# Kernel tuning notes

Hardware: AMD Instinct MI355X
Metric: run time of the kernel (lower is better)

The kernel has to match this reference:

```python
import jax, jax.numpy as jnp
import numpy as np
from jax.ops import segment_sum, segment_max

N = 20000      # nodes
DEG = 16       # incoming edges per node
E = N * DEG    # edges
IN = 128       # in_features
BOND = 16      # bond_features_dim
OUT = 128      # output_features
NUM_LAYERS = 3
LEAKY = 0.2
ELU_ALPHA = 1.0


def _lin_params(key, out_f, in_f):
    kw, kb = jax.random.split(key)
    s = 1.0 / np.sqrt(in_f)
    w = jax.random.uniform(kw, (out_f, in_f), jnp.float32, -s, s)
    b = jax.random.uniform(kb, (out_f,), jnp.float32, -s, s)
    return w, b


def setup_inputs() -> dict:
    key = jax.random.key(0)
    ks = jax.random.split(key, 20)
    atom_features = jax.random.normal(ks[0], (N, IN), jnp.float32)
    edge_src = jax.random.randint(ks[1], (E,), 0, N, jnp.int32)
    # every node receives exactly DEG edges (avoids the isolated-node bug path)
    edge_dst = jnp.repeat(jnp.arange(N, dtype=jnp.int32), DEG)
    bond_features = jax.random.normal(ks[2], (E, BOND), jnp.float32)

    v1_fc1_w, v1_fc1_b = _lin_params(ks[3], OUT, IN)
    v1_fc2_w, v1_fc2_b = _lin_params(ks[4], OUT, IN + BOND)
    v1_att_w, v1_att_b = _lin_params(ks[5], 1, 2 * OUT)
    v1_attend_w, v1_attend_b = _lin_params(ks[6], OUT, OUT)
    v1_gru_wih, v1_gru_bih = _lin_params(ks[7], 3 * OUT, OUT)
    v1_gru_whh, v1_gru_bhh = _lin_params(ks[8], 3 * OUT, OUT)

    v2_fc1_w, v2_fc1_b = _lin_params(ks[9], 1, 2 * OUT)
    v2_fc2_w, v2_fc2_b = _lin_params(ks[10], OUT, OUT)
    v2_gru_wih, v2_gru_bih = _lin_params(ks[11], 3 * OUT, OUT)
    v2_gru_whh, v2_gru_bhh = _lin_params(ks[12], 3 * OUT, OUT)

    lin_w, lin_b = _lin_params(ks[13], OUT, OUT)

    return dict(atom_features=atom_features, edge_src=edge_src, edge_dst=edge_dst,
                bond_features=bond_features,
                v1_fc1_w=v1_fc1_w, v1_fc1_b=v1_fc1_b, v1_fc2_w=v1_fc2_w, v1_fc2_b=v1_fc2_b,
                v1_att_w=v1_att_w, v1_att_b=v1_att_b, v1_attend_w=v1_attend_w, v1_attend_b=v1_attend_b,
                v1_gru_wih=v1_gru_wih, v1_gru_whh=v1_gru_whh, v1_gru_bih=v1_gru_bih, v1_gru_bhh=v1_gru_bhh,
                v2_fc1_w=v2_fc1_w, v2_fc1_b=v2_fc1_b, v2_fc2_w=v2_fc2_w, v2_fc2_b=v2_fc2_b,
                v2_gru_wih=v2_gru_wih, v2_gru_whh=v2_gru_whh, v2_gru_bih=v2_gru_bih, v2_gru_bhh=v2_gru_bhh,
                lin_w=lin_w, lin_b=lin_b)


def _linear(x, w, b):
    return x @ w.T + b


def _gru_cell(x, h, wih, whh, bih, bhh):
    gi = x @ wih.T + bih   # [N, 3*OUT]
    gh = h @ whh.T + bhh
    i_r, i_z, i_n = jnp.split(gi, 3, axis=-1)
    h_r, h_z, h_n = jnp.split(gh, 3, axis=-1)
    r = jax.nn.sigmoid(i_r + h_r)
    z = jax.nn.sigmoid(i_z + h_z)
    n = jnp.tanh(i_n + r * h_n)
    return (1.0 - z) * n + z * h


def _segment_softmax(logits, seg, n):
    m = segment_max(logits, seg, num_segments=n)
    ex = jnp.exp(logits - m[seg])
    den = segment_sum(ex, seg, num_segments=n)
    return ex / den[seg]


def reference(atom_features, edge_src, edge_dst, bond_features,
              v1_fc1_w, v1_fc1_b, v1_fc2_w, v1_fc2_b, v1_att_w, v1_att_b,
              v1_attend_w, v1_attend_b, v1_gru_wih, v1_gru_whh, v1_gru_bih, v1_gru_bhh,
              v2_fc1_w, v2_fc1_b, v2_fc2_w, v2_fc2_b,
              v2_gru_wih, v2_gru_whh, v2_gru_bih, v2_gru_bhh,
              lin_w, lin_b):
    n = atom_features.shape[0]
    lrelu = lambda x: jax.nn.leaky_relu(x, negative_slope=LEAKY)

    # ---- GATlayerV1 ----
    new_atom = lrelu(_linear(atom_features, v1_fc1_w, v1_fc1_b))           # [N, OUT]
    nbr_trans = _linear(new_atom, v1_attend_w, v1_attend_b)                # [N, OUT]
    nbr_in = jnp.concatenate([atom_features[edge_src], bond_features], axis=1)  # [E, IN+BOND]
    nbr = lrelu(_linear(nbr_in, v1_fc2_w, v1_fc2_b))                       # [E, OUT]
    pair = jnp.concatenate([new_atom[edge_dst], nbr], axis=1)              # [E, 2*OUT]
    logits = lrelu(_linear(pair, v1_att_w, v1_att_b))[:, 0]                # [E]
    score = _segment_softmax(logits, edge_dst, n)                          # [E]
    transform = segment_sum(score[:, None] * nbr_trans[edge_src], edge_dst, num_segments=n)
    ctx = jax.nn.elu(transform, alpha=ELU_ALPHA)
    h = _gru_cell(ctx, new_atom, v1_gru_wih, v1_gru_whh, v1_gru_bih, v1_gru_bhh)
    G_0 = new_atom

    all_tensors = [h]

    # ---- GATlayerV2 (shared weights across layers 2..NUM_LAYERS) ----
    for _ in range(NUM_LAYERS - 1):
        nt = _linear(h, v2_fc2_w, v2_fc2_b)                                # [N, OUT]
        pair2 = jnp.concatenate([h[edge_dst], h[edge_src]], axis=1)        # [E, 2*OUT]
        lg = lrelu(_linear(pair2, v2_fc1_w, v2_fc1_b))[:, 0]               # [E]
        sc = _segment_softmax(lg, edge_dst, n)
        tr = segment_sum(sc[:, None] * nt[edge_src], edge_dst, num_segments=n)
        ctx2 = jax.nn.elu(tr, alpha=ELU_ALPHA)
        h = _gru_cell(ctx2, h, v2_gru_wih, v2_gru_whh, v2_gru_bih, v2_gru_bhh)
        all_tensors.append(h)

    all_stack = jnp.stack(all_tensors)           # [NUM_LAYERS, N, OUT]
    averaged = all_stack.mean(axis=0)            # [N, OUT]
    output = jax.nn.gelu(_linear(averaged, lin_w, lin_b), approximate=False)
    return (output, all_stack, G_0, averaged)
```

## Files before the change

kernel.cpp:

```cpp
#include <hip/hip_runtime.h>
#include <math.h>

#define NN 20000
#define EE 320000

using short8 = __attribute__((ext_vector_type(8))) short;
using f32x4  = __attribute__((ext_vector_type(4))) float;
using u16x4  = __attribute__((ext_vector_type(4))) unsigned short;

__device__ __forceinline__ unsigned short f2bf(float x) {
    union { float f; unsigned u; } v; v.f = x;
    unsigned r = (v.u + 0x7fffu + ((v.u >> 16) & 1u)) >> 16;
    return (unsigned short)r;
}
__device__ __forceinline__ float bf2f(unsigned short b) {
    union { unsigned u; float f; } v; v.u = ((unsigned)b) << 16;
    return v.f;
}
__device__ __forceinline__ float sigmoidf_(float x) { return 1.f / (1.f + __expf(-x)); }
__device__ __forceinline__ float tanhf_(float x) {
    float e = __expf(-2.f * x);
    return (1.f - e) / (1.f + e);
}
__device__ __forceinline__ float lrelu_(float x) { return x > 0.f ? x : 0.2f * x; }
__device__ __forceinline__ float elu_(float x) { return x > 0.f ? x : __expf(x) - 1.f; }

struct PackDesc { const float* w; unsigned short* out; int O; int ldw; int mode; };
struct PackArgs { PackDesc d[10]; };

__global__ void k_pack(PackArgs args) {
    PackDesc d = args.d[blockIdx.y];
    int idx = blockIdx.x * 256 + threadIdx.x;
    if (d.mode == 1) {
        if (idx >= 512) return;
        int t = idx >> 6, l = idx & 63;
        int lr = l & 15, lg = l >> 4;
        int ch = lr * 8 + t;
        short8 o;
        #pragma unroll
        for (int j = 0; j < 8; j++) {
            int k = lg * 8 + j;
            o[j] = (k < 16) ? (short)f2bf(d.w[(size_t)ch * 144 + 128 + k]) : (short)0;
        }
        *(short8*)(d.out + (size_t)idx * 8) = o;
        return;
    }
    int total = (d.O / 16) * 4 * 64;
    if (idx >= total) return;
    int l = idx & 63, rest = idx >> 6;
    int ko = rest & 3, no = rest >> 2;
    int row = no * 16 + (l & 15);
    int col0 = ko * 32 + ((l >> 4) * 8);
    const float* src = d.w + (size_t)row * d.ldw + col0;
    unsigned short o[8];
    #pragma unroll
    for (int j = 0; j < 8; j++) o[j] = f2bf(src[j]);
    #pragma unroll
    for (int j = 0; j < 8; j++) d.out[(size_t)idx * 8 + j] = o[j];
}

__global__ __launch_bounds__(256) void k_v1_front(
    const float* __restrict__ atom,
    const unsigned short* __restrict__ Bfc1, const unsigned short* __restrict__ BW2a,
    const float* __restrict__ fc1_b, const float* __restrict__ fc2_b,
    const float* __restrict__ attw,
    float* __restrict__ g0, unsigned short* __restrict__ naBf,
    unsigned short* __restrict__ Ubf, float* __restrict__ adst)
{
    __shared__ float Xs[16][132];
    __shared__ unsigned short Ys2[16 * 128];
    const int tid = threadIdx.x, l = tid & 63, w = tid >> 6;
    const int lr = l & 15, lg = l >> 4;
    const int m0 = blockIdx.x * 16;

    f32x4 acc1[2] = {}, accU[2] = {};
    #pragma unroll
    for (int ko = 0; ko < 4; ko++) {
        const f32x4* ap = (const f32x4*)(atom + (size_t)(m0 + lr) * 128 + ko * 32 + lg * 8);
        f32x4 a0 = ap[0], a1 = ap[1];
        short8 af;
        #pragma unroll
        for (int j = 0; j < 4; j++) { af[j] = (short)f2bf(a0[j]); af[4 + j] = (short)f2bf(a1[j]); }
        #pragma unroll
        for (int i = 0; i < 2; i++) {
            int t = w * 2 + i;
            short8 b1 = *(const short8*)(Bfc1 + ((size_t)(t * 4 + ko) * 64 + l) * 8);
            acc1[i] = __builtin_amdgcn_mfma_f32_16x16x32_bf16(af, b1, acc1[i], 0, 0, 0);
            short8 bu = *(const short8*)(BW2a + ((size_t)(t * 4 + ko) * 64 + l) * 8);
            accU[i] = __builtin_amdgcn_mfma_f32_16x16x32_bf16(af, bu, accU[i], 0, 0, 0);
        }
    }
    #pragma unroll
    for (int i = 0; i < 2; i++) {
        int col = (w * 2 + i) * 16 + lr;
        float b1v = fc1_b[col], bUv = fc2_b[col];
        #pragma unroll
        for (int r = 0; r < 4; r++) {
            int row = lg * 4 + r;
            float v = lrelu_(acc1[i][r] + b1v);
            Xs[row][col] = v;
            Ys2[row * 128 + col] = f2bf(accU[i][r] + bUv);
        }
    }
    __syncthreads();
    *(short8*)(Ubf + (size_t)m0 * 128 + tid * 8) = *(const short8*)(Ys2 + tid * 8);
    {
        int row = tid >> 4, q = tid & 15;
        short8 tmp;
        float p = 0.f;
        float vv[8];
        #pragma unroll
        for (int j = 0; j < 8; j++) {
            float x = Xs[row][q * 8 + j];
            vv[j] = x;
            tmp[j] = (short)f2bf(x);
            p = fmaf(x, attw[q * 8 + j], p);
        }
        *(f32x4*)(g0 + (size_t)(m0 + row) * 128 + q * 8) = *(f32x4*)vv;
        *(f32x4*)(g0 + (size_t)(m0 + row) * 128 + q * 8 + 4) = *(f32x4*)(vv + 4);
        *(short8*)(naBf + (size_t)(m0 + row) * 128 + q * 8) = tmp;
        #pragma unroll
        for (int m = 1; m <= 8; m <<= 1) p += __shfl_xor(p, m, 16);
        if (q == 0) adst[m0 + row] = p;
    }
}

__global__ __launch_bounds__(256) void k_logits_v1(
    const unsigned short* __restrict__ U, const int* __restrict__ esrc,
    const float* __restrict__ bond, const unsigned short* __restrict__ BW2b,
    const float* __restrict__ attw, const float* __restrict__ attb1,
    const float* __restrict__ adst, float* __restrict__ logits)
{
    const int tid = threadIdx.x, l = tid & 63, w = tid >> 6;
    const int lr = l & 15, lg = l >> 4;
    const int n = blockIdx.x * 4 + w;
    const int e0 = n * 16;

    short8 af = {};
    if (lg < 2) {
        const f32x4* bp = (const f32x4*)(bond + (size_t)(e0 + lr) * 16 + lg * 8);
        f32x4 b0 = bp[0], b1 = bp[1];
        #pragma unroll
        for (int j = 0; j < 4; j++) { af[j] = (short)f2bf(b0[j]); af[4 + j] = (short)f2bf(b1[j]); }
    }
    f32x4 c[8];
    #pragma unroll
    for (int t = 0; t < 8; t++) {
        short8 bf = *(const short8*)(BW2b + (size_t)(t * 64 + l) * 8);
        f32x4 z = {};
        c[t] = __builtin_amdgcn_mfma_f32_16x16x32_bf16(af, bf, z, 0, 0, 0);
    }
    float aw[8];
    #pragma unroll
    for (int t = 0; t < 8; t++) aw[t] = attw[128 + lr * 8 + t];

    float s[4];
    #pragma unroll
    for (int r = 0; r < 4; r++) {
        int e = e0 + lg * 4 + r;
        int src = esrc[e];
        short8 u = *(const short8*)(U + (size_t)src * 128 + lr * 8);
        float a0 = 0.f;
        #pragma unroll
        for (int t = 0; t < 8; t++)
            a0 = fmaf(aw[t], lrelu_(c[t][r] + bf2f((unsigned short)u[t])), a0);
        s[r] = a0;
    }
    #pragma unroll
    for (int mk = 1; mk <= 8; mk <<= 1)
        #pragma unroll
        for (int r = 0; r < 4; r++) s[r] += __shfl_xor(s[r], mk, 16);
    if (lr == 0) {
        float anode = adst[n], ab = attb1[0];
        f32x4 o;
        #pragma unroll
        for (int r = 0; r < 4; r++) o[r] = lrelu_(anode + ab + s[r]);
        *(f32x4*)(logits + e0 + lg * 4) = o;
    }
}

template<int AGGMODE, int FRONT, int FINAL>
__global__ __launch_bounds__(512, 4) void k_gru(
    const float* __restrict__ logits, const float* __restrict__ aD,
    const float* __restrict__ bS, const float* __restrict__ b1,
    const int* __restrict__ esrc, const unsigned short* __restrict__ V,
    const unsigned short* __restrict__ Bpre, const float* __restrict__ bpre,
    const unsigned short* __restrict__ Bih, const unsigned short* __restrict__ Bhh,
    const float* __restrict__ bih, const float* __restrict__ bhh,
    const unsigned short* __restrict__ hprevBf, float* __restrict__ houtF,
    unsigned short* __restrict__ houtBf,
    const float* __restrict__ w2att, float* __restrict__ aDOut, float* __restrict__ bSOut,
    const float* __restrict__ as0, const float* __restrict__ as1,
    const unsigned short* __restrict__ Blin, const float* __restrict__ linb,
    float* __restrict__ avgOut, float* __restrict__ outF)
{
    __shared__ unsigned short aggS[32][136];
    __shared__ unsigned short ctxS[32][136];
    __shared__ unsigned short hpS[32][136];
    __shared__ float hoS[32][132];
    const int tid = threadIdx.x, l = tid & 63, w = tid >> 6;
    const int lr = l & 15, lg = l >> 4;
    const int m0 = blockIdx.x * 32;
    const int srow = tid >> 4, sc0 = (tid & 15) * 8;

    *(short8*)&hpS[srow][sc0] = *(const short8*)(hprevBf + (size_t)(m0 + srow) * 128 + sc0);

    {
        const int q = tid & 15;
        const int gnode = m0 + srow;
        const int e = gnode * 16 + q;
        const int src = esrc[e];
        float lgt;
        if (AGGMODE == 0) lgt = logits[e];
        else              lgt = lrelu_(aD[gnode] + bS[src] + b1[0]);
        float mx = lgt;
        #pragma unroll
        for (int mk = 1; mk <= 8; mk <<= 1) mx = fmaxf(mx, __shfl_xor(mx, mk, 16));
        float ex = __expf(lgt - mx);
        float den = ex;
        #pragma unroll
        for (int mk = 1; mk <= 8; mk <<= 1) den += __shfl_xor(den, mk, 16);
        float wq = ex / den;
        float s[8] = {};
        #pragma unroll
        for (int i = 0; i < 16; i++) {
            float wi = __shfl(wq, i, 16);
            int si = __shfl(src, i, 16);
            const unsigned short* vp = V + (size_t)si * 128 + q * 4;
            u16x4 v0 = *(const u16x4*)vp;
            #pragma unroll
            for (int j = 0; j < 4; j++) s[j] = fmaf(wi, bf2f(v0[j]), s[j]);
            u16x4 v1 = *(const u16x4*)(vp + 64);
            #pragma unroll
            for (int j = 0; j < 4; j++) s[4 + j] = fmaf(wi, bf2f(v1[j]), s[4 + j]);
        }
        u16x4 o0, o1;
        #pragma unroll
        for (int j = 0; j < 4; j++) { o0[j] = f2bf(s[j]); o1[j] = f2bf(s[4 + j]); }
        *(u16x4*)&aggS[srow][q * 4] = o0;
        *(u16x4*)&aggS[srow][64 + q * 4] = o1;
    }
    __syncthreads();

    f32x4 accp[2] = {};
    #pragma unroll
    for (int ko = 0; ko < 4; ko++) {
        short8 bf = *(const short8*)(Bpre + ((size_t)(w * 4 + ko) * 64 + l) * 8);
        #pragma unroll
        for (int rt = 0; rt < 2; rt++) {
            short8 af = *(const short8*)&aggS[rt * 16 + lr][ko * 32 + lg * 8];
            accp[rt] = __builtin_amdgcn_mfma_f32_16x16x32_bf16(af, bf, accp[rt], 0, 0, 0);
        }
    }
    {
        const int col = w * 16 + lr;
        const float bb = bpre[col];
        #pragma unroll
        for (int rt = 0; rt < 2; rt++)
            #pragma unroll
            for (int r = 0; r < 4; r++)
                ctxS[rt * 16 + lg * 4 + r][col] = f2bf(elu_(accp[rt][r] + bb));
    }
    __syncthreads();

    f32x4 ai[2][3] = {}, ah[2][3] = {};
    #pragma unroll
    for (int ko = 0; ko < 4; ko++) {
        short8 afc[2], afh[2];
        #pragma unroll
        for (int rt = 0; rt < 2; rt++) {
            afc[rt] = *(const short8*)&ctxS[rt * 16 + lr][ko * 32 + lg * 8];
            afh[rt] = *(const short8*)&hpS[rt * 16 + lr][ko * 32 + lg * 8];
        }
        #pragma unroll
        for (int g = 0; g < 3; g++) {
            short8 bi = *(const short8*)(Bih + ((size_t)((w + 8 * g) * 4 + ko) * 64 + l) * 8);
            #pragma unroll
            for (int rt = 0; rt < 2; rt++)
                ai[rt][g] = __builtin_amdgcn_mfma_f32_16x16x32_bf16(afc[rt], bi, ai[rt][g], 0, 0, 0);
            short8 bh = *(const short8*)(Bhh + ((size_t)((w + 8 * g) * 4 + ko) * 64 + l) * 8);
            #pragma unroll
            for (int rt = 0; rt < 2; rt++)
                ah[rt][g] = __builtin_amdgcn_mfma_f32_16x16x32_bf16(afh[rt], bh, ah[rt][g], 0, 0, 0);
        }
    }
    __syncthreads();

    {
        const int c = w * 16 + lr;
        const float br = bih[c] + bhh[c];
        const float bz = bih[c + 128] + bhh[c + 128];
        const float bin_ = bih[c + 256];
        const float bhn = bhh[c + 256];
        #pragma unroll
        for (int rt = 0; rt < 2; rt++)
            #pragma unroll
            for (int r = 0; r < 4; r++) {
                const int lrow = rt * 16 + lg * 4 + r;
                float rg = sigmoidf_(ai[rt][0][r] + ah[rt][0][r] + br);
                float zg = sigmoidf_(ai[rt][1][r] + ah[rt][1][r] + bz);
                float ng = tanhf_(ai[rt][2][r] + bin_ + rg * (ah[rt][2][r] + bhn));
                float hp = bf2f(hpS[lrow][c]);
                hoS[lrow][c] = fmaf(zg, hp - ng, ng);
            }
    }
    __syncthreads();

    {
        float v[8];
        #pragma unroll
        for (int k = 0; k < 8; k++) v[k] = hoS[srow][sc0 + k];
        f32x4* dst = (f32x4*)(houtF + (size_t)(m0 + srow) * 128 + sc0);
        dst[0] = *(f32x4*)v;
        dst[1] = *(f32x4*)(v + 4);
        if (FINAL == 0) {
            short8 p;
            #pragma unroll
            for (int k = 0; k < 8; k++) p[k] = (short)f2bf(v[k]);
            *(short8*)(houtBf + (size_t)(m0 + srow) * 128 + sc0) = p;
        }
    }

    if (FRONT) {
        int row = tid >> 4, q = tid & 15;
        float pa = 0.f, pb = 0.f;
        #pragma unroll
        for (int j = 0; j < 8; j++) {
            float x = hoS[row][q * 8 + j];
            pa = fmaf(x, w2att[q * 8 + j], pa);
            pb = fmaf(x, w2att[128 + q * 8 + j], pb);
        }
        #pragma unroll
        for (int m = 1; m <= 8; m <<= 1) {
            pa += __shfl_xor(pa, m, 16);
            pb += __shfl_xor(pb, m, 16);
        }
        if (q == 0) { aDOut[m0 + row] = pa; bSOut[m0 + row] = pb; }
    }

    if (FINAL) {
        {
            const f32x4* p0 = (const f32x4*)(as0 + (size_t)(m0 + srow) * 128 + sc0);
            const f32x4* p1 = (const f32x4*)(as1 + (size_t)(m0 + srow) * 128 + sc0);
            f32x4* pav = (f32x4*)(avgOut + (size_t)(m0 + srow) * 128 + sc0);
            #pragma unroll
            for (int k = 0; k < 2; k++) {
                f32x4 x0 = p0[k], x1 = p1[k];
                f32x4 av;
                #pragma unroll
                for (int j = 0; j < 4; j++)
                    av[j] = (x0[j] + x1[j] + hoS[srow][sc0 + k * 4 + j]) * (1.f / 3.f);
                pav[k] = av;
                #pragma unroll
                for (int j = 0; j < 4; j++) ctxS[srow][sc0 + k * 4 + j] = f2bf(av[j]);
            }
        }
        __syncthreads();
        f32x4 acc2[2] = {};
        #pragma unroll
        for (int ko = 0; ko < 4; ko++) {
            short8 bf = *(const short8*)(Blin + ((size_t)(w * 4 + ko) * 64 + l) * 8);
            #pragma unroll
            for (int rt = 0; rt < 2; rt++) {
                short8 af = *(const short8*)&ctxS[rt * 16 + lr][ko * 32 + lg * 8];
                acc2[rt] = __builtin_amdgcn_mfma_f32_16x16x32_bf16(af, bf, acc2[rt], 0, 0, 0);
            }
        }
        {
            const int col = w * 16 + lr;
            const float bb = linb[col];
            #pragma unroll
            for (int rt = 0; rt < 2; rt++)
                #pragma unroll
                for (int r = 0; r < 4; r++) {
                    float vv = acc2[rt][r] + bb;
                    hoS[rt * 16 + lg * 4 + r][col] =
                        0.5f * vv * (1.f + erff(vv * 0.70710678118654752f));
                }
        }
        __syncthreads();
        {
            float v[8];
            #pragma unroll
            for (int k = 0; k < 8; k++) v[k] = hoS[srow][sc0 + k];
            f32x4* dst = (f32x4*)(outF + (size_t)(m0 + srow) * 128 + sc0);
            dst[0] = *(f32x4*)v;
            dst[1] = *(f32x4*)(v + 4);
        }
    }
}

extern "C" void kernel_launch(void* const* d_in, const int* in_sizes, int n_in,
                              void* d_out, int out_size, void* d_ws, size_t ws_size,
                              hipStream_t stream) {
    const float* atom     = (const float*)d_in[0];
    const int*   esrc     = (const int*)d_in[1];
    const float* bond     = (const float*)d_in[3];
    const float* fc1_w    = (const float*)d_in[4];
    const float* fc1_b    = (const float*)d_in[5];
    const float* fc2_w    = (const float*)d_in[6];
    const float* fc2_b    = (const float*)d_in[7];
    const float* att_w    = (const float*)d_in[8];
    const float* att_b    = (const float*)d_in[9];
    const float* attend_w = (const float*)d_in[10];
    const float* attend_b = (const float*)d_in[11];
    const float* gih1     = (const float*)d_in[12];
    const float* ghh1     = (const float*)d_in[13];
    const float* bih1     = (const float*)d_in[14];
    const float* bhh1     = (const float*)d_in[15];
    const float* fc1v2_w  = (const float*)d_in[16];
    const float* fc1v2_b  = (const float*)d_in[17];
    const float* fc2v2_w  = (const float*)d_in[18];
    const float* fc2v2_b  = (const float*)d_in[19];
    const float* gih2     = (const float*)d_in[20];
    const float* ghh2     = (const float*)d_in[21];
    const float* bih2     = (const float*)d_in[22];
    const float* bhh2     = (const float*)d_in[23];
    const float* lin_w    = (const float*)d_in[24];
    const float* lin_b    = (const float*)d_in[25];

    char* wsb = (char*)d_ws;
    size_t off = 0;
    auto allocB = [&](size_t bytes) {
        size_t o = off; off = (off + bytes + 255) & ~(size_t)255; return o;
    };
    unsigned short* Bfc1   = (unsigned short*)(wsb + allocB(128 * 128 * 2));
    unsigned short* Batt   = (unsigned short*)(wsb + allocB(128 * 128 * 2));
    unsigned short* BW2a   = (unsigned short*)(wsb + allocB(128 * 128 * 2));
    unsigned short* BW2b   = (unsigned short*)(wsb + allocB(512 * 8 * 2));
    unsigned short* Bgih1  = (unsigned short*)(wsb + allocB(384 * 128 * 2));
    unsigned short* Bghh1  = (unsigned short*)(wsb + allocB(384 * 128 * 2));
    unsigned short* Bfc2v2 = (unsigned short*)(wsb + allocB(128 * 128 * 2));
    unsigned short* Bgih2  = (unsigned short*)(wsb + allocB(384 * 128 * 2));
    unsigned short* Bghh2  = (unsigned short*)(wsb + allocB(384 * 128 * 2));
    unsigned short* Blin   = (unsigned short*)(wsb + allocB(128 * 128 * 2));
    unsigned short* naBf   = (unsigned short*)(wsb + allocB((size_t)NN * 128 * 2));
    unsigned short* Ubf    = (unsigned short*)(wsb + allocB((size_t)NN * 128 * 2));
    unsigned short* h1Bf   = (unsigned short*)(wsb + allocB((size_t)NN * 128 * 2));
    unsigned short* h2Bf   = (unsigned short*)(wsb + allocB((size_t)NN * 128 * 2));
    float* logits = (float*)(wsb + allocB((size_t)EE * 4));
    float* adst   = (float*)(wsb + allocB((size_t)NN * 4));
    float* aD     = (float*)(wsb + allocB((size_t)NN * 4));
    float* bS     = (float*)(wsb + allocB((size_t)NN * 4));
    (void)ws_size;

    float* out0 = (float*)d_out;
    float* as0  = out0 + (size_t)NN * 128;
    float* as1  = as0 + (size_t)NN * 128;
    float* as2  = as1 + (size_t)NN * 128;
    float* g0   = out0 + (size_t)4 * NN * 128;
    float* avg  = out0 + (size_t)5 * NN * 128;

    PackArgs pa;
    pa.d[0] = { fc1_w,    Bfc1,   128, 128, 0 };
    pa.d[1] = { attend_w, Batt,   128, 128, 0 };
    pa.d[2] = { fc2_w,    BW2a,   128, 144, 0 };
    pa.d[3] = { gih1,     Bgih1,  384, 128, 0 };
    pa.d[4] = { ghh1,     Bghh1,  384, 128, 0 };
    pa.d[5] = { fc2v2_w,  Bfc2v2, 128, 128, 0 };
    pa.d[6] = { gih2,     Bgih2,  384, 128, 0 };
    pa.d[7] = { ghh2,     Bghh2,  384, 128, 0 };
    pa.d[8] = { lin_w,    Blin,   128, 128, 0 };
    pa.d[9] = { fc2_w,    BW2b,   0,   0,   1 };
    k_pack<<<dim3(24, 10), 256, 0, stream>>>(pa);

    const int GB = NN / 16;
    const int GB32 = NN / 32;

    k_v1_front<<<GB, 256, 0, stream>>>(atom, Bfc1, BW2a, fc1_b, fc2_b, att_w,
                                       g0, naBf, Ubf, adst);
    k_logits_v1<<<NN / 4, 256, 0, stream>>>(Ubf, esrc, bond, BW2b, att_w, att_b,
                                            adst, logits);
    k_gru<0, 1, 0><<<GB32, 512, 0, stream>>>(
        logits, nullptr, nullptr, nullptr, esrc, naBf,
        Batt, attend_b,
        Bgih1, Bghh1, bih1, bhh1, naBf, as0, h1Bf,
        fc1v2_w, aD, bS,
        nullptr, nullptr, nullptr, nullptr, nullptr, nullptr);

    k_gru<1, 1, 0><<<GB32, 512, 0, stream>>>(
        nullptr, aD, bS, fc1v2_b, esrc, h1Bf,
        Bfc2v2, fc2v2_b,
        Bgih2, Bghh2, bih2, bhh2, h1Bf, as1, h2Bf,
        fc1v2_w, aD, bS,
        nullptr, nullptr, nullptr, nullptr, nullptr, nullptr);

    k_gru<1, 0, 1><<<GB32, 512, 0, stream>>>(
        nullptr, aD, bS, fc1v2_b, esrc, h2Bf,
        Bfc2v2, fc2v2_b,
        Bgih2, Bghh2, bih2, bhh2, h2Bf, as2, nullptr,
        nullptr, nullptr, nullptr,
        as0, as1, Blin, lin_b, avg, out0);
}
```

Before: 126.7 us.

## Fuse V1 edge-logit kernel into first GRU kernel and hoist Whh MFMAs

Removes the separate k_logits_v1 launch and its E-sized logits buffer by computing the bond-feature MFMA and attention logits inside the first GRU kernel, keeping them in shared memory. It also moves the hidden-state (Whh) MFMAs into the same loop as the pre-aggregation projection, so they no longer wait behind the ctx barrier, and it drops one barrier while adding another in the final path. This saves a launch and a global round trip for the logits, at the cost of more work per GRU block and higher register pressure at 512 threads.

```diff
diff --git a/kernel.cpp b/kernel.cpp
--- a/kernel.cpp
+++ b/kernel.cpp
@@ -125,64 +125,12 @@
     }
 }
 
-__global__ __launch_bounds__(256) void k_logits_v1(
-    const unsigned short* __restrict__ U, const int* __restrict__ esrc,
+template<int AGGMODE, int FRONT, int FINAL>
+__global__ __launch_bounds__(512, 4) void k_gru(
+    const float* __restrict__ aD, const float* __restrict__ bS, const float* __restrict__ b1,
     const float* __restrict__ bond, const unsigned short* __restrict__ BW2b,
     const float* __restrict__ attw, const float* __restrict__ attb1,
-    const float* __restrict__ adst, float* __restrict__ logits)
-{
-    const int tid = threadIdx.x, l = tid & 63, w = tid >> 6;
-    const int lr = l & 15, lg = l >> 4;
-    const int n = blockIdx.x * 4 + w;
-    const int e0 = n * 16;
-
-    short8 af = {};
-    if (lg < 2) {
-        const f32x4* bp = (const f32x4*)(bond + (size_t)(e0 + lr) * 16 + lg * 8);
-        f32x4 b0 = bp[0], b1 = bp[1];
-        #pragma unroll
-        for (int j = 0; j < 4; j++) { af[j] = (short)f2bf(b0[j]); af[4 + j] = (short)f2bf(b1[j]); }
-    }
-    f32x4 c[8];
-    #pragma unroll
-    for (int t = 0; t < 8; t++) {
-        short8 bf = *(const short8*)(BW2b + (size_t)(t * 64 + l) * 8);
-        f32x4 z = {};
-        c[t] = __builtin_amdgcn_mfma_f32_16x16x32_bf16(af, bf, z, 0, 0, 0);
-    }
-    float aw[8];
-    #pragma unroll
-    for (int t = 0; t < 8; t++) aw[t] = attw[128 + lr * 8 + t];
-
-    float s[4];
-    #pragma unroll
-    for (int r = 0; r < 4; r++) {
-        int e = e0 + lg * 4 + r;
-        int src = esrc[e];
-        short8 u = *(const short8*)(U + (size_t)src * 128 + lr * 8);
-        float a0 = 0.f;
-        #pragma unroll
-        for (int t = 0; t < 8; t++)
-            a0 = fmaf(aw[t], lrelu_(c[t][r] + bf2f((unsigned short)u[t])), a0);
-        s[r] = a0;
-    }
-    #pragma unroll
-    for (int mk = 1; mk <= 8; mk <<= 1)
-        #pragma unroll
-        for (int r = 0; r < 4; r++) s[r] += __shfl_xor(s[r], mk, 16);
-    if (lr == 0) {
-        float anode = adst[n], ab = attb1[0];
-        f32x4 o;
-        #pragma unroll
-        for (int r = 0; r < 4; r++) o[r] = lrelu_(anode + ab + s[r]);
-        *(f32x4*)(logits + e0 + lg * 4) = o;
-    }
-}
-
-template<int AGGMODE, int FRONT, int FINAL>
-__global__ __launch_bounds__(512, 4) void k_gru(
-    const float* __restrict__ logits, const float* __restrict__ aD,
-    const float* __restrict__ bS, const float* __restrict__ b1,
+    const float* __restrict__ adst, const unsigned short* __restrict__ U,
     const int* __restrict__ esrc, const unsigned short* __restrict__ V,
     const unsigned short* __restrict__ Bpre, const float* __restrict__ bpre,
     const unsigned short* __restrict__ Bih, const unsigned short* __restrict__ Bhh,
@@ -198,12 +146,64 @@
     __shared__ unsigned short ctxS[32][136];
     __shared__ unsigned short hpS[32][136];
     __shared__ float hoS[32][132];
+    __shared__ float lgS[32][16];
     const int tid = threadIdx.x, l = tid & 63, w = tid >> 6;
     const int lr = l & 15, lg = l >> 4;
     const int m0 = blockIdx.x * 32;
     const int srow = tid >> 4, sc0 = (tid & 15) * 8;
 
     *(short8*)&hpS[srow][sc0] = *(const short8*)(hprevBf + (size_t)(m0 + srow) * 128 + sc0);
+
+    if (AGGMODE == 0) {
+        float aw[8];
+        #pragma unroll
+        for (int t = 0; t < 8; t++) aw[t] = attw[128 + lr * 8 + t];
+        const float ab = attb1[0];
+        #pragma unroll
+        for (int nn = 0; nn < 4; nn++) {
+            const int n = m0 + w * 4 + nn;
+            const int e0 = n * 16;
+            short8 af = {};
+            if (lg < 2) {
+                const f32x4* bp = (const f32x4*)(bond + (size_t)(e0 + lr) * 16 + lg * 8);
+                f32x4 b0 = bp[0], b1v = bp[1];
+                #pragma unroll
+                for (int j = 0; j < 4; j++) {
+                    af[j] = (short)f2bf(b0[j]); af[4 + j] = (short)f2bf(b1v[j]);
+                }
+            }
+            f32x4 c[8];
+            #pragma unroll
+            for (int t = 0; t < 8; t++) {
+                short8 bw = *(const short8*)(BW2b + (size_t)(t * 64 + l) * 8);
+                f32x4 z = {};
+                c[t] = __builtin_amdgcn_mfma_f32_16x16x32_bf16(af, bw, z, 0, 0, 0);
+            }
+            float s[4];
+            #pragma unroll
+            for (int r = 0; r < 4; r++) {
+                int e = e0 + lg * 4 + r;
+                int src = esrc[e];
+                short8 u = *(const short8*)(U + (size_t)src * 128 + lr * 8);
+                float a0 = 0.f;
+                #pragma unroll
+                for (int t = 0; t < 8; t++)
+                    a0 = fmaf(aw[t], lrelu_(c[t][r] + bf2f((unsigned short)u[t])), a0);
+                s[r] = a0;
+            }
+            #pragma unroll
+            for (int mk = 1; mk <= 8; mk <<= 1)
+                #pragma unroll
+                for (int r = 0; r < 4; r++) s[r] += __shfl_xor(s[r], mk, 16);
+            if (lr == 0) {
+                float anode = adst[n];
+                #pragma unroll
+                for (int r = 0; r < 4; r++)
+                    lgS[w * 4 + nn][lg * 4 + r] = lrelu_(anode + ab + s[r]);
+            }
+        }
+        __syncthreads();
+    }
 
     {
         const int q = tid & 15;
@@ -211,7 +211,7 @@
         const int e = gnode * 16 + q;
         const int src = esrc[e];
         float lgt;
-        if (AGGMODE == 0) lgt = logits[e];
+        if (AGGMODE == 0) lgt = lgS[srow][q];
         else              lgt = lrelu_(aD[gnode] + bS[src] + b1[0]);
         float mx = lgt;
         #pragma unroll
@@ -243,13 +243,25 @@
     __syncthreads();
 
     f32x4 accp[2] = {};
+    f32x4 ah[2][3] = {};
     #pragma unroll
     for (int ko = 0; ko < 4; ko++) {
-        short8 bf = *(const short8*)(Bpre + ((size_t)(w * 4 + ko) * 64 + l) * 8);
+        short8 afA[2], afh[2];
         #pragma unroll
         for (int rt = 0; rt < 2; rt++) {
-            short8 af = *(const short8*)&aggS[rt * 16 + lr][ko * 32 + lg * 8];
-            accp[rt] = __builtin_amdgcn_mfma_f32_16x16x32_bf16(af, bf, accp[rt], 0, 0, 0);
+            afA[rt] = *(const short8*)&aggS[rt * 16 + lr][ko * 32 + lg * 8];
+            afh[rt] = *(const short8*)&hpS[rt * 16 + lr][ko * 32 + lg * 8];
+        }
+        short8 bfp = *(const short8*)(Bpre + ((size_t)(w * 4 + ko) * 64 + l) * 8);
+        #pragma unroll
+        for (int rt = 0; rt < 2; rt++)
+            accp[rt] = __builtin_amdgcn_mfma_f32_16x16x32_bf16(afA[rt], bfp, accp[rt], 0, 0, 0);
+        #pragma unroll
+        for (int g = 0; g < 3; g++) {
+            short8 bh = *(const short8*)(Bhh + ((size_t)((w + 8 * g) * 4 + ko) * 64 + l) * 8);
+            #pragma unroll
+            for (int rt = 0; rt < 2; rt++)
+                ah[rt][g] = __builtin_amdgcn_mfma_f32_16x16x32_bf16(afh[rt], bh, ah[rt][g], 0, 0, 0);
         }
     }
     {
@@ -263,29 +275,21 @@
     }
     __syncthreads();
 
-    f32x4 ai[2][3] = {}, ah[2][3] = {};
+    f32x4 ai[2][3] = {};
     #pragma unroll
     for (int ko = 0; ko < 4; ko++) {
-        short8 afc[2], afh[2];
-        #pragma unroll
-        for (int rt = 0; rt < 2; rt++) {
+        short8 afc[2];
+        #pragma unroll
+        for (int rt = 0; rt < 2; rt++)
             afc[rt] = *(const short8*)&ctxS[rt * 16 + lr][ko * 32 + lg * 8];
-            afh[rt] = *(const short8*)&hpS[rt * 16 + lr][ko * 32 + lg * 8];
-        }
         #pragma unroll
         for (int g = 0; g < 3; g++) {
             short8 bi = *(const short8*)(Bih + ((size_t)((w + 8 * g) * 4 + ko) * 64 + l) * 8);
             #pragma unroll
             for (int rt = 0; rt < 2; rt++)
                 ai[rt][g] = __builtin_amdgcn_mfma_f32_16x16x32_bf16(afc[rt], bi, ai[rt][g], 0, 0, 0);
-            short8 bh = *(const short8*)(Bhh + ((size_t)((w + 8 * g) * 4 + ko) * 64 + l) * 8);
-            #pragma unroll
-            for (int rt = 0; rt < 2; rt++)
-                ah[rt][g] = __builtin_amdgcn_mfma_f32_16x16x32_bf16(afh[rt], bh, ah[rt][g], 0, 0, 0);
-        }
-    }
-    __syncthreads();
-
+        }
+    }
     {
         const int c = w * 16 + lr;
         const float br = bih[c] + bhh[c];
@@ -366,6 +370,7 @@
                 acc2[rt] = __builtin_amdgcn_mfma_f32_16x16x32_bf16(af, bf, acc2[rt], 0, 0, 0);
             }
         }
+        __syncthreads();
         {
             const int col = w * 16 + lr;
             const float bb = linb[col];
@@ -438,7 +443,6 @@
     unsigned short* Ubf    = (unsigned short*)(wsb + allocB((size_t)NN * 128 * 2));
     unsigned short* h1Bf   = (unsigned short*)(wsb + allocB((size_t)NN * 128 * 2));
     unsigned short* h2Bf   = (unsigned short*)(wsb + allocB((size_t)NN * 128 * 2));
-    float* logits = (float*)(wsb + allocB((size_t)EE * 4));
     float* adst   = (float*)(wsb + allocB((size_t)NN * 4));
     float* aD     = (float*)(wsb + allocB((size_t)NN * 4));
     float* bS     = (float*)(wsb + allocB((size_t)NN * 4));
@@ -469,24 +473,28 @@
 
     k_v1_front<<<GB, 256, 0, stream>>>(atom, Bfc1, BW2a, fc1_b, fc2_b, att_w,
                                        g0, naBf, Ubf, adst);
-    k_logits_v1<<<NN / 4, 256, 0, stream>>>(Ubf, esrc, bond, BW2b, att_w, att_b,
-                                            adst, logits);
     k_gru<0, 1, 0><<<GB32, 512, 0, stream>>>(
-        logits, nullptr, nullptr, nullptr, esrc, naBf,
+        nullptr, nullptr, nullptr,
+        bond, BW2b, att_w, att_b, adst, Ubf,
+        esrc, naBf,
         Batt, attend_b,
         Bgih1, Bghh1, bih1, bhh1, naBf, as0, h1Bf,
         fc1v2_w, aD, bS,
         nullptr, nullptr, nullptr, nullptr, nullptr, nullptr);
 
     k_gru<1, 1, 0><<<GB32, 512, 0, stream>>>(
-        nullptr, aD, bS, fc1v2_b, esrc, h1Bf,
+        aD, bS, fc1v2_b,
+        nullptr, nullptr, nullptr, nullptr, nullptr, nullptr,
+        esrc, h1Bf,
         Bfc2v2, fc2v2_b,
         Bgih2, Bghh2, bih2, bhh2, h1Bf, as1, h2Bf,
         fc1v2_w, aD, bS,
         nullptr, nullptr, nullptr, nullptr, nullptr, nullptr);
 
     k_gru<1, 0, 1><<<GB32, 512, 0, stream>>>(
-        nullptr, aD, bS, fc1v2_b, esrc, h2Bf,
+        aD, bS, fc1v2_b,
+        nullptr, nullptr, nullptr, nullptr, nullptr, nullptr,
+        esrc, h2Bf,
         Bfc2v2, fc2v2_b,
         Bgih2, Bghh2, bih2, bhh2, h2Bf, as2, nullptr,
         nullptr, nullptr, nullptr,
```

After: 123.3 us. 2.7% less time.
